# Performance work log

Hardware: AMD Instinct MI355X
Metric: run time of the kernel (lower is better)

## Reference

```python
import jax, jax.numpy as jnp
import numpy as np

N = 2048
D_IN = 128
D_OUT = 128
H = 8
EDGE_DIM = 8
EDGE_HID = 32
NEG_SLOPE = 0.2


def setup_inputs() -> dict:
    key = jax.random.key(0)
    ks = jax.random.split(key, 9)
    return {
        "inputs": jax.random.normal(ks[0], (N, D_IN), dtype=jnp.float32),
        "adj": jax.random.randint(ks[1], (N, N), 0, 2, dtype=jnp.int32),
        "edge_attr": jax.random.normal(ks[2], (N, N, EDGE_DIM), dtype=jnp.float32),
        # Linear weights stored as [in, out] (y = x @ W)
        "Wq": jax.random.normal(ks[3], (D_IN, D_OUT), dtype=jnp.float32) * 0.05,
        "Wk": jax.random.normal(ks[4], (D_IN, D_OUT), dtype=jnp.float32) * 0.05,
        "Wv": jax.random.normal(ks[5], (D_IN, D_OUT), dtype=jnp.float32) * 0.05,
        "We": jax.random.normal(ks[6], (EDGE_DIM, EDGE_HID), dtype=jnp.float32) * 0.05,
        "Wr": jax.random.normal(ks[7], (EDGE_HID, D_OUT), dtype=jnp.float32) * 0.05,
        "Wo": jax.random.normal(ks[8], (D_OUT, D_OUT), dtype=jnp.float32) * 0.05,
    }


def reference(inputs, adj, edge_attr, Wq, Wk, Wv, We, Wr, Wo):
    n = inputs.shape[0]
    dh = D_OUT // H  # head dim = 16
    # Projections -> [H, N, dh]
    Q = (inputs @ Wq).reshape(n, H, dh).transpose(1, 0, 2)
    K = (inputs @ Wk).reshape(n, H, dh).transpose(1, 0, 2)
    V = (inputs @ Wv).reshape(n, H, dh).transpose(1, 0, 2)
    # Edge bias: r_ij = W_r(W_e(e_ij)) viewed per-head; bias_hij = q_hi . r_ijh.
    # Fold We@Wr and contract with Q first to avoid materializing [N,N,D_OUT].
    Wer = (We @ Wr).reshape(EDGE_DIM, H, dh)          # [E, H, dh]
    QW = jnp.einsum('hid,ehd->hie', Q, Wer)           # [H, N, E]
    scores = (jnp.einsum('hid,hjd->hij', Q, K)
              + jnp.einsum('hie,ije->hij', QW, edge_attr)) / jnp.sqrt(jnp.float32(dh))
    scores = jax.nn.leaky_relu(scores, NEG_SLOPE)
    # Adjacency mask: only attend along existing edges
    scores = jnp.where((adj > 0)[None, :, :], scores, jnp.float32(-1e9))
    attn = jax.nn.softmax(scores, axis=-1)            # dropout is identity in eval
    out = jnp.einsum('hij,hjd->hid', attn, V)         # [H, N, dh]
    out = out.transpose(1, 0, 2).reshape(n, D_OUT)
    return out @ Wo
```

## Files before the change

### kernel.cpp

```cpp
#include <hip/hip_runtime.h>
#include <math.h>

#define NN 2048
#define DD 128
#define HH 8
#define DHH 16
#define EDIM 8
#define EHID 32

typedef __attribute__((address_space(1))) const void GV;
typedef __attribute__((address_space(3))) void LV;

__global__ __launch_bounds__(384) void proj_kernel(
    const float* __restrict__ X,
    const float* __restrict__ Wq, const float* __restrict__ Wk,
    const float* __restrict__ Wv, const float* __restrict__ We,
    const float* __restrict__ Wr,
    float* __restrict__ Qo, float* __restrict__ Ko,
    float* __restrict__ Vo, float* __restrict__ QWo) {
  __shared__ float x_lds[2][128];
  __shared__ float wer_lds[8][128];
  __shared__ float q_lds[2][128];
  const int t = threadIdx.x;
  const int i0 = blockIdx.x * 2;

  if (t < 256) x_lds[t >> 7][t & 127] = X[(size_t)i0 * 128 + t];

  if (t < 128) {
    float acc[EDIM];
#pragma unroll
    for (int e = 0; e < EDIM; ++e) acc[e] = 0.f;
    for (int k = 0; k < EHID; ++k) {
      const float wr = Wr[k * 128 + t];
#pragma unroll
      for (int e = 0; e < EDIM; ++e) acc[e] = fmaf(We[e * EHID + k], wr, acc[e]);
    }
#pragma unroll
    for (int e = 0; e < EDIM; ++e) wer_lds[e][t] = acc[e];
  }
  __syncthreads();

  const int mat = t >> 7;
  const int c = t & 127;
  const float* __restrict__ W = (mat == 0) ? Wq : ((mat == 1) ? Wk : Wv);
  float a0 = 0.f, a1 = 0.f;
#pragma unroll 8
  for (int d = 0; d < 128; ++d) {
    const float w = W[d * 128 + c];
    a0 = fmaf(x_lds[0][d], w, a0);
    a1 = fmaf(x_lds[1][d], w, a1);
  }
  float* __restrict__ Out = (mat == 0) ? Qo : ((mat == 1) ? Ko : Vo);
  Out[(size_t)i0 * 128 + c] = a0;
  Out[(size_t)(i0 + 1) * 128 + c] = a1;
  if (mat == 0) { q_lds[0][c] = a0; q_lds[1][c] = a1; }
  __syncthreads();

  if (t < 64) {
    const int h = t >> 3, e = t & 7;
#pragma unroll
    for (int r = 0; r < 2; ++r) {
      float s = 0.f;
#pragma unroll
      for (int d = 0; d < DHH; ++d)
        s = fmaf(q_lds[r][h * DHH + d], wer_lds[e][h * DHH + d], s);
      QWo[(size_t)(i0 + r) * 64 + h * 8 + e] = s;
    }
  }
}

__global__ __launch_bounds__(320) void attn_kernel(
    const float* __restrict__ Qg, const float* __restrict__ Kg,
    const float* __restrict__ Vg, const float* __restrict__ QWg,
    const int* __restrict__ adj, const float* __restrict__ Eg,
    const float* __restrict__ Wo, float* __restrict__ out) {
  __shared__ float4 Ks_lds[4][512];
  __shared__ float4 Vs_lds[4][512];
  __shared__ float4 Es_lds[4][64];
  __shared__ float mbuf[128 * 18];
  __shared__ float o_lds[2][128];

  const int t = threadIdx.x;
  const int i0 = blockIdx.x * 2;

  if (t >= 256) {
    const int lid = t - 256;
    const int hi = lid >> 5;
    const int r = lid & 31;
    const int h_p = r & 7, qq_p = r >> 3;
    const float* Kbase = Kg + (size_t)hi * 16384 + h_p * 16 + qq_p * 4;
    const float* Vbase = Vg + (size_t)hi * 16384 + h_p * 16 + qq_p * 4;
    const int il_e = lid >> 5;
    const int jo_e = (lid & 31) >> 1, half = lid & 1;
    const float* Ebase = Eg + ((size_t)(i0 + il_e) * 2048 + jo_e * 128) * 8 + half * 4;

    auto ISSUE = [&](int slot, int jj) {
      const float* kb = Kbase + (size_t)jj * 128;
      const float* vb = Vbase + (size_t)jj * 128;
      const float* eb = Ebase + (size_t)jj * 8;
#pragma unroll
      for (int j = 0; j < 8; ++j)
        __builtin_amdgcn_global_load_lds((GV*)(kb + j * 32768),
                                         (LV*)&Ks_lds[slot][j * 64], 16, 0, 0);
#pragma unroll
      for (int j = 0; j < 8; ++j)
        __builtin_amdgcn_global_load_lds((GV*)(vb + j * 32768),
                                         (LV*)&Vs_lds[slot][j * 64], 16, 0, 0);
      __builtin_amdgcn_global_load_lds((GV*)eb, (LV*)&Es_lds[slot][0], 16, 0, 0);
    };

    ISSUE(0, 0); ISSUE(1, 1); ISSUE(2, 2);
    asm volatile("s_waitcnt vmcnt(34)" ::: "memory");
    __builtin_amdgcn_s_barrier();
    __builtin_amdgcn_sched_barrier(0);
    for (int jj = 0; jj < 128; ++jj) {
      if (jj < 125) {
        ISSUE((jj + 3) & 3, jj + 3);
        asm volatile("s_waitcnt vmcnt(34)" ::: "memory");
      } else if (jj == 125) {
        asm volatile("s_waitcnt vmcnt(17)" ::: "memory");
      } else {
        asm volatile("s_waitcnt vmcnt(0)" ::: "memory");
      }
      __builtin_amdgcn_s_barrier();
      __builtin_amdgcn_sched_barrier(0);
    }
  } else {
    const int il = t & 1;
    const int h = (t >> 1) & 7;
    const int jo = t >> 4;
    const int i = i0 + il;

    float4 q0, q1, q2, q3, qw0, qw1;
    {
      const float4* qp = (const float4*)(Qg + (size_t)i * 128 + h * 16);
      q0 = qp[0]; q1 = qp[1]; q2 = qp[2]; q3 = qp[3];
      const float4* wp = (const float4*)(QWg + (size_t)i * 64 + h * 8);
      qw0 = wp[0]; qw1 = wp[1];
    }

    float acc[16];
#pragma unroll
    for (int d = 0; d < 16; ++d) acc[d] = 0.f;
    float m = -INFINITY, mt = -INFINITY, l = 0.f;

    const int4* __restrict__ ap4 = (const int4*)(adj + (size_t)i * NN + jo * 128);

    auto score = [&](const float4 E0, const float4 E1,
                     const float4 K0, const float4 K1, const float4 K2,
                     const float4 K3, const int a) -> float {
      float s0 = q0.x * K0.x;    s0 = fmaf(q0.y, K0.y, s0);
      s0 = fmaf(q0.z, K0.z, s0); s0 = fmaf(q0.w, K0.w, s0);
      s0 = fmaf(q1.x, K1.x, s0); s0 = fmaf(q1.y, K1.y, s0);
      s0 = fmaf(q1.z, K1.z, s0); s0 = fmaf(q1.w, K1.w, s0);
      float s1 = q2.x * K2.x;    s1 = fmaf(q2.y, K2.y, s1);
      s1 = fmaf(q2.z, K2.z, s1); s1 = fmaf(q2.w, K2.w, s1);
      s1 = fmaf(q3.x, K3.x, s1); s1 = fmaf(q3.y, K3.y, s1);
      s1 = fmaf(q3.z, K3.z, s1); s1 = fmaf(q3.w, K3.w, s1);
      float b0 = qw0.x * E0.x;    b0 = fmaf(qw0.y, E0.y, b0);
      b0 = fmaf(qw0.z, E0.z, b0); b0 = fmaf(qw0.w, E0.w, b0);
      b0 = fmaf(qw1.x, E1.x, b0); b0 = fmaf(qw1.y, E1.y, b0);
      b0 = fmaf(qw1.z, E1.z, b0); b0 = fmaf(qw1.w, E1.w, b0);
      const float raw = (s0 + s1) + b0;
      float sc2 = fmaf(0.14426950f, fabsf(raw), 0.21640425f * raw);
      sc2 = (a > 0) ? sc2 : -1e9f;
      if (sc2 > mt) {
        const float rr = exp2f(m - sc2);
        l *= rr;
#pragma unroll
        for (int d = 0; d < 16; ++d) acc[d] *= rr;
        m = sc2; mt = sc2 + 12.f;
      }
      const float p = exp2f(sc2 - m);
      l += p;
      return p;
    };
    auto pv = [&](const float p, const float4 V0, const float4 V1,
                  const float4 V2, const float4 V3) {
      acc[0]  = fmaf(p, V0.x, acc[0]);  acc[1]  = fmaf(p, V0.y, acc[1]);
      acc[2]  = fmaf(p, V0.z, acc[2]);  acc[3]  = fmaf(p, V0.w, acc[3]);
      acc[4]  = fmaf(p, V1.x, acc[4]);  acc[5]  = fmaf(p, V1.y, acc[5]);
      acc[6]  = fmaf(p, V1.z, acc[6]);  acc[7]  = fmaf(p, V1.w, acc[7]);
      acc[8]  = fmaf(p, V2.x, acc[8]);  acc[9]  = fmaf(p, V2.y, acc[9]);
      acc[10] = fmaf(p, V2.z, acc[10]); acc[11] = fmaf(p, V2.w, acc[11]);
      acc[12] = fmaf(p, V3.x, acc[12]); acc[13] = fmaf(p, V3.y, acc[13]);
      acc[14] = fmaf(p, V3.z, acc[14]); acc[15] = fmaf(p, V3.w, acc[15]);
    };

    int4 a_cur = ap4[0];
    __builtin_amdgcn_s_barrier();
    __builtin_amdgcn_sched_barrier(0);

    for (int j4 = 0; j4 < 32; ++j4) {
      const int4 a_nxt = ap4[j4 < 31 ? j4 + 1 : 31];
#pragma unroll
      for (int u4 = 0; u4 < 4; ++u4) {
        const int jj = j4 * 4 + u4;
        const int slot = jj & 3;
        const int a = (u4 == 0) ? a_cur.x : (u4 == 1) ? a_cur.y
                    : (u4 == 2) ? a_cur.z : a_cur.w;
        const float4* kq = &Ks_lds[slot][jo * 32 + h];
        const float4 K0 = kq[0], K1 = kq[8], K2 = kq[16], K3 = kq[24];
        const float4* vq = &Vs_lds[slot][jo * 32 + h];
        const float4 V0 = vq[0], V1 = vq[8], V2 = vq[16], V3 = vq[24];
        const float4* eq = &Es_lds[slot][il * 32 + jo * 2];
        const float4 E0 = eq[0], E1 = eq[1];
        const float p = score(E0, E1, K0, K1, K2, K3, a);
        pv(p, V0, V1, V2, V3);
        __builtin_amdgcn_s_barrier();
        __builtin_amdgcn_sched_barrier(0);
      }
      a_cur = a_nxt;
    }

    {
      const int u = t & 15;
      (void)u;
    }
    __syncthreads();
    const int u = t & 15;
    for (int k = 8; k >= 1; k >>= 1) {
      if (jo >= k && jo < 2 * k) {
        float* b = mbuf + ((size_t)((jo - k) * 16 + u)) * 18;
        b[0] = m; b[1] = l;
#pragma unroll
        for (int d = 0; d < 16; ++d) b[2 + d] = acc[d];
      }
      __syncthreads();
      if (jo < k) {
        const float* b = mbuf + ((size_t)(jo * 16 + u)) * 18;
        const float m2 = b[0], l2 = b[1];
        const float M = fmaxf(m, m2);
        const float sa = exp2f(m - M), sb = exp2f(m2 - M);
        l = l * sa + l2 * sb;
#pragma unroll
        for (int d = 0; d < 16; ++d) acc[d] = acc[d] * sa + b[2 + d] * sb;
        m = M;
      }
      __syncthreads();
    }
    if (jo == 0) {
      const float inv = 1.f / l;
#pragma unroll
      for (int d = 0; d < 16; ++d) o_lds[il][h * 16 + d] = acc[d] * inv;
    }
    __syncthreads();
    const int r = t >> 7, c = t & 127;
    float s = 0.f;
#pragma unroll 8
    for (int d = 0; d < 128; ++d)
      s = fmaf(o_lds[r][d], Wo[d * 128 + c], s);
    out[(size_t)(i0 + r) * 128 + c] = s;
    return;
  }

  __syncthreads();
  for (int k = 8; k >= 1; k >>= 1) { __syncthreads(); __syncthreads(); }
  __syncthreads();
}

extern "C" void kernel_launch(void* const* d_in, const int* in_sizes, int n_in,
                              void* d_out, int out_size, void* d_ws, size_t ws_size,
                              hipStream_t stream) {
  const float* X   = (const float*)d_in[0];
  const int*   adj = (const int*)d_in[1];
  const float* E   = (const float*)d_in[2];
  const float* Wq  = (const float*)d_in[3];
  const float* Wk  = (const float*)d_in[4];
  const float* Wv  = (const float*)d_in[5];
  const float* We  = (const float*)d_in[6];
  const float* Wr  = (const float*)d_in[7];
  const float* Wo  = (const float*)d_in[8];
  float* out = (float*)d_out;

  float* Qs  = (float*)d_ws;
  float* Ks  = Qs + (size_t)NN * DD;
  float* Vs  = Ks + (size_t)NN * DD;
  float* QWs = Vs + (size_t)NN * DD;

  hipLaunchKernelGGL(proj_kernel, dim3(NN / 2), dim3(384), 0, stream,
                     X, Wq, Wk, Wv, We, Wr, Qs, Ks, Vs, QWs);
  hipLaunchKernelGGL(attn_kernel, dim3(NN / 2), dim3(320), 0, stream,
                     Qs, Ks, Vs, QWs, adj, E, Wo, out);
}
```

Baseline: 360.7 us.

## Process four query rows per attention block with deeper LDS ring and staged adjacency

The attention kernel now handles four query rows per block instead of two, halving the grid and doubling reuse of each K/V tile staged in LDS. The producer wave group uses a six-slot ring with 256 steps of 8 keys each, and also stages the adjacency row into LDS via direct global-to-LDS loads. Reads are XOR-swizzled to avoid bank conflicts, and the merge and output projection are restructured for the new 8-way key split. This cuts K/V global traffic per query and removes per-thread adjacency loads, at the cost of twice as many barriers per pass and fewer blocks for occupancy.

```diff
diff --git a/kernel.cpp b/kernel.cpp
--- a/kernel.cpp
+++ b/kernel.cpp
@@ -3,13 +3,16 @@
 
 #define NN 2048
 #define DD 128
-#define HH 8
-#define DHH 16
 #define EDIM 8
 #define EHID 32
+#define DHH 16
 
 typedef __attribute__((address_space(1))) const void GV;
 typedef __attribute__((address_space(3))) void LV;
+
+#define NB 6
+#define NSTEP 256
+#define RROWS 4
 
 __global__ __launch_bounds__(384) void proj_kernel(
     const float* __restrict__ X,
@@ -69,98 +72,120 @@
   }
 }
 
+#define DOT4ADD(S, A, B) do {            \
+    S = fmaf((A).x, (B).x, S);           \
+    S = fmaf((A).y, (B).y, S);           \
+    S = fmaf((A).z, (B).z, S);           \
+    S = fmaf((A).w, (B).w, S); } while (0)
+
 __global__ __launch_bounds__(320) void attn_kernel(
     const float* __restrict__ Qg, const float* __restrict__ Kg,
     const float* __restrict__ Vg, const float* __restrict__ QWg,
     const int* __restrict__ adj, const float* __restrict__ Eg,
     const float* __restrict__ Wo, float* __restrict__ out) {
-  __shared__ float4 Ks_lds[4][512];
-  __shared__ float4 Vs_lds[4][512];
-  __shared__ float4 Es_lds[4][64];
-  __shared__ float mbuf[128 * 18];
-  __shared__ float o_lds[2][128];
+  __shared__ float4 KL[NB][256];
+  __shared__ float4 VL[NB][256];
+  __shared__ float4 EL[NB][64];
+  __shared__ int    AL[NB][64];
+  __shared__ float  mbuf[128 * 18];
+  __shared__ float  o_lds[4][128];
 
   const int t = threadIdx.x;
-  const int i0 = blockIdx.x * 2;
+  const int i0 = blockIdx.x * RROWS;
+
+  float acc[16];
+#pragma unroll
+  for (int d = 0; d < 16; ++d) acc[d] = 0.f;
+  float m = -INFINITY, mt = -INFINITY, l = 0.f;
 
   if (t >= 256) {
-    const int lid = t - 256;
-    const int hi = lid >> 5;
-    const int r = lid & 31;
-    const int h_p = r & 7, qq_p = r >> 3;
-    const float* Kbase = Kg + (size_t)hi * 16384 + h_p * 16 + qq_p * 4;
-    const float* Vbase = Vg + (size_t)hi * 16384 + h_p * 16 + qq_p * 4;
-    const int il_e = lid >> 5;
-    const int jo_e = (lid & 31) >> 1, half = lid & 1;
-    const float* Ebase = Eg + ((size_t)(i0 + il_e) * 2048 + jo_e * 128) * 8 + half * 4;
-
-    auto ISSUE = [&](int slot, int jj) {
-      const float* kb = Kbase + (size_t)jj * 128;
-      const float* vb = Vbase + (size_t)jj * 128;
-      const float* eb = Ebase + (size_t)jj * 8;
-#pragma unroll
-      for (int j = 0; j < 8; ++j)
-        __builtin_amdgcn_global_load_lds((GV*)(kb + j * 32768),
-                                         (LV*)&Ks_lds[slot][j * 64], 16, 0, 0);
-#pragma unroll
-      for (int j = 0; j < 8; ++j)
-        __builtin_amdgcn_global_load_lds((GV*)(vb + j * 32768),
-                                         (LV*)&Vs_lds[slot][j * 64], 16, 0, 0);
-      __builtin_amdgcn_global_load_lds((GV*)eb, (LV*)&Es_lds[slot][0], 16, 0, 0);
+    const int ln = t - 256;
+    const float* kS = Kg + (size_t)(ln >> 5) * 128 + (ln & 31) * 4;
+    const float* vS = Vg + (size_t)(ln >> 5) * 128 + (ln & 31) * 4;
+    const float* eS = Eg + ((size_t)(i0 + (ln >> 4)) * NN + ((ln >> 1) & 7)) * 8
+                         + (ln & 1) * 4;
+    const int jsA = ((ln & 15) > 7) ? 7 : (ln & 15);
+    const int* aS = adj + (size_t)(i0 + (ln >> 4)) * NN + jsA;
+
+    auto ISSUE = [&](int sl, int j0) {
+#pragma unroll
+      for (int p = 0; p < 4; ++p)
+        __builtin_amdgcn_global_load_lds((GV*)(kS + (size_t)(j0 + p * 2) * 128),
+                                         (LV*)&KL[sl][p * 64], 16, 0, 0);
+#pragma unroll
+      for (int p = 0; p < 4; ++p)
+        __builtin_amdgcn_global_load_lds((GV*)(vS + (size_t)(j0 + p * 2) * 128),
+                                         (LV*)&VL[sl][p * 64], 16, 0, 0);
+      __builtin_amdgcn_global_load_lds((GV*)(eS + (size_t)j0 * 8),
+                                       (LV*)&EL[sl][0], 16, 0, 0);
+      __builtin_amdgcn_global_load_lds((GV*)(aS + j0), (LV*)&AL[sl][0], 4, 0, 0);
     };
 
-    ISSUE(0, 0); ISSUE(1, 1); ISSUE(2, 2);
-    asm volatile("s_waitcnt vmcnt(34)" ::: "memory");
+    ISSUE(0, 0); ISSUE(1, 8); ISSUE(2, 16); ISSUE(3, 24); ISSUE(4, 32);
+    asm volatile("s_waitcnt vmcnt(40)" ::: "memory");
+    __builtin_amdgcn_sched_barrier(0);
     __builtin_amdgcn_s_barrier();
-    __builtin_amdgcn_sched_barrier(0);
-    for (int jj = 0; jj < 128; ++jj) {
-      if (jj < 125) {
-        ISSUE((jj + 3) & 3, jj + 3);
-        asm volatile("s_waitcnt vmcnt(34)" ::: "memory");
-      } else if (jj == 125) {
-        asm volatile("s_waitcnt vmcnt(17)" ::: "memory");
+
+    int ip = 5, jI = 40;
+    for (int s = 0; s < NSTEP; ++s) {
+      if (s <= 250) {
+        ISSUE(ip, jI);
+        jI += 8;
+        if (++ip == NB) ip = 0;
+        asm volatile("s_waitcnt vmcnt(40)" ::: "memory");
+      } else if (s == 251) {
+        asm volatile("s_waitcnt vmcnt(30)" ::: "memory");
+      } else if (s == 252) {
+        asm volatile("s_waitcnt vmcnt(20)" ::: "memory");
+      } else if (s == 253) {
+        asm volatile("s_waitcnt vmcnt(10)" ::: "memory");
       } else {
         asm volatile("s_waitcnt vmcnt(0)" ::: "memory");
       }
+      __builtin_amdgcn_sched_barrier(0);
       __builtin_amdgcn_s_barrier();
-      __builtin_amdgcn_sched_barrier(0);
     }
   } else {
-    const int il = t & 1;
-    const int h = (t >> 1) & 7;
-    const int jo = t >> 4;
+    const int il = t & 3;
+    const int h = (t >> 2) & 7;
+    const int js = t >> 5;
+    const int hs = (h >> 1) & 3;
+    const int hb = il & 1;
     const int i = i0 + il;
 
-    float4 q0, q1, q2, q3, qw0, qw1;
+    float4 qq0, qq1, qq2, qq3, qw0, qw1;
     {
       const float4* qp = (const float4*)(Qg + (size_t)i * 128 + h * 16);
-      q0 = qp[0]; q1 = qp[1]; q2 = qp[2]; q3 = qp[3];
+      qq0 = qp[0 ^ hs]; qq1 = qp[1 ^ hs]; qq2 = qp[2 ^ hs]; qq3 = qp[3 ^ hs];
       const float4* wp = (const float4*)(QWg + (size_t)i * 64 + h * 8);
-      qw0 = wp[0]; qw1 = wp[1];
-    }
-
-    float acc[16];
-#pragma unroll
-    for (int d = 0; d < 16; ++d) acc[d] = 0.f;
-    float m = -INFINITY, mt = -INFINITY, l = 0.f;
-
-    const int4* __restrict__ ap4 = (const int4*)(adj + (size_t)i * NN + jo * 128);
-
-    auto score = [&](const float4 E0, const float4 E1,
-                     const float4 K0, const float4 K1, const float4 K2,
-                     const float4 K3, const int a) -> float {
-      float s0 = q0.x * K0.x;    s0 = fmaf(q0.y, K0.y, s0);
-      s0 = fmaf(q0.z, K0.z, s0); s0 = fmaf(q0.w, K0.w, s0);
-      s0 = fmaf(q1.x, K1.x, s0); s0 = fmaf(q1.y, K1.y, s0);
-      s0 = fmaf(q1.z, K1.z, s0); s0 = fmaf(q1.w, K1.w, s0);
-      float s1 = q2.x * K2.x;    s1 = fmaf(q2.y, K2.y, s1);
-      s1 = fmaf(q2.z, K2.z, s1); s1 = fmaf(q2.w, K2.w, s1);
-      s1 = fmaf(q3.x, K3.x, s1); s1 = fmaf(q3.y, K3.y, s1);
-      s1 = fmaf(q3.z, K3.z, s1); s1 = fmaf(q3.w, K3.w, s1);
-      float b0 = qw0.x * E0.x;    b0 = fmaf(qw0.y, E0.y, b0);
-      b0 = fmaf(qw0.z, E0.z, b0); b0 = fmaf(qw0.w, E0.w, b0);
-      b0 = fmaf(qw1.x, E1.x, b0); b0 = fmaf(qw1.y, E1.y, b0);
-      b0 = fmaf(qw1.z, E1.z, b0); b0 = fmaf(qw1.w, E1.w, b0);
+      qw0 = wp[0 ^ hb]; qw1 = wp[1 ^ hb];
+    }
+
+    const int kOff = js * 32 + h * 4;
+    const int eOff = il * 16 + js * 2;
+    const int aOff = il * 16 + js;
+
+    __builtin_amdgcn_s_barrier();
+    __builtin_amdgcn_sched_barrier(0);
+
+    int sl = 0;
+    for (int s = 0; s < NSTEP; ++s) {
+      const int a = AL[sl][aOff];
+      const float4 kk0 = KL[sl][kOff + (0 ^ hs)];
+      const float4 kk1 = KL[sl][kOff + (1 ^ hs)];
+      const float4 kk2 = KL[sl][kOff + (2 ^ hs)];
+      const float4 kk3 = KL[sl][kOff + (3 ^ hs)];
+      const float4 ee0 = EL[sl][eOff + (0 ^ hb)];
+      const float4 ee1 = EL[sl][eOff + (1 ^ hb)];
+      const float4 vv0 = VL[sl][kOff + (0 ^ hs)];
+      const float4 vv1 = VL[sl][kOff + (1 ^ hs)];
+      const float4 vv2 = VL[sl][kOff + (2 ^ hs)];
+      const float4 vv3 = VL[sl][kOff + (3 ^ hs)];
+
+      float s0 = 0.f, s1 = 0.f, b0 = 0.f;
+      DOT4ADD(s0, qq0, kk0); DOT4ADD(s0, qq1, kk1);
+      DOT4ADD(s1, qq2, kk2); DOT4ADD(s1, qq3, kk3);
+      DOT4ADD(b0, qw0, ee0); DOT4ADD(b0, qw1, ee1);
       const float raw = (s0 + s1) + b0;
       float sc2 = fmaf(0.14426950f, fabsf(raw), 0.21640425f * raw);
       sc2 = (a > 0) ? sc2 : -1e9f;
@@ -173,90 +198,70 @@
       }
       const float p = exp2f(sc2 - m);
       l += p;
-      return p;
-    };
-    auto pv = [&](const float p, const float4 V0, const float4 V1,
-                  const float4 V2, const float4 V3) {
-      acc[0]  = fmaf(p, V0.x, acc[0]);  acc[1]  = fmaf(p, V0.y, acc[1]);
-      acc[2]  = fmaf(p, V0.z, acc[2]);  acc[3]  = fmaf(p, V0.w, acc[3]);
-      acc[4]  = fmaf(p, V1.x, acc[4]);  acc[5]  = fmaf(p, V1.y, acc[5]);
-      acc[6]  = fmaf(p, V1.z, acc[6]);  acc[7]  = fmaf(p, V1.w, acc[7]);
-      acc[8]  = fmaf(p, V2.x, acc[8]);  acc[9]  = fmaf(p, V2.y, acc[9]);
-      acc[10] = fmaf(p, V2.z, acc[10]); acc[11] = fmaf(p, V2.w, acc[11]);
-      acc[12] = fmaf(p, V3.x, acc[12]); acc[13] = fmaf(p, V3.y, acc[13]);
-      acc[14] = fmaf(p, V3.z, acc[14]); acc[15] = fmaf(p, V3.w, acc[15]);
-    };
-
-    int4 a_cur = ap4[0];
-    __builtin_amdgcn_s_barrier();
-    __builtin_amdgcn_sched_barrier(0);
-
-    for (int j4 = 0; j4 < 32; ++j4) {
-      const int4 a_nxt = ap4[j4 < 31 ? j4 + 1 : 31];
-#pragma unroll
-      for (int u4 = 0; u4 < 4; ++u4) {
-        const int jj = j4 * 4 + u4;
-        const int slot = jj & 3;
-        const int a = (u4 == 0) ? a_cur.x : (u4 == 1) ? a_cur.y
-                    : (u4 == 2) ? a_cur.z : a_cur.w;
-        const float4* kq = &Ks_lds[slot][jo * 32 + h];
-        const float4 K0 = kq[0], K1 = kq[8], K2 = kq[16], K3 = kq[24];
-        const float4* vq = &Vs_lds[slot][jo * 32 + h];
-        const float4 V0 = vq[0], V1 = vq[8], V2 = vq[16], V3 = vq[24];
-        const float4* eq = &Es_lds[slot][il * 32 + jo * 2];
-        const float4 E0 = eq[0], E1 = eq[1];
-        const float p = score(E0, E1, K0, K1, K2, K3, a);
-        pv(p, V0, V1, V2, V3);
-        __builtin_amdgcn_s_barrier();
-        __builtin_amdgcn_sched_barrier(0);
-      }
-      a_cur = a_nxt;
-    }
-
-    {
-      const int u = t & 15;
-      (void)u;
+      acc[0]  = fmaf(p, vv0.x, acc[0]);  acc[1]  = fmaf(p, vv0.y, acc[1]);
+      acc[2]  = fmaf(p, vv0.z, acc[2]);  acc[3]  = fmaf(p, vv0.w, acc[3]);
+      acc[4]  = fmaf(p, vv1.x, acc[4]);  acc[5]  = fmaf(p, vv1.y, acc[5]);
+      acc[6]  = fmaf(p, vv1.z, acc[6]);  acc[7]  = fmaf(p, vv1.w, acc[7]);
+      acc[8]  = fmaf(p, vv2.x, acc[8]);  acc[9]  = fmaf(p, vv2.y, acc[9]);
+      acc[10] = fmaf(p, vv2.z, acc[10]); acc[11] = fmaf(p, vv2.w, acc[11]);
+      acc[12] = fmaf(p, vv3.x, acc[12]); acc[13] = fmaf(p, vv3.y, acc[13]);
+      acc[14] = fmaf(p, vv3.z, acc[14]); acc[15] = fmaf(p, vv3.w, acc[15]);
+
+      __builtin_amdgcn_sched_barrier(0);
+      __builtin_amdgcn_s_barrier();
+      __builtin_amdgcn_sched_barrier(0);
+      if (++sl == NB) sl = 0;
+    }
+  }
+
+  const int ilc = t & 3, hc = (t >> 2) & 7, jsc = t >> 5;
+  const int hsc = (hc >> 1) & 3;
+  const int u = t & 31;
+  for (int k = 4; k >= 1; k >>= 1) {
+    if (t < 256 && jsc >= k && jsc < 2 * k) {
+      float* b = mbuf + ((size_t)((jsc - k) * 32 + u)) * 18;
+      b[0] = m; b[1] = l;
+#pragma unroll
+      for (int d = 0; d < 16; ++d) b[2 + d] = acc[d];
     }
     __syncthreads();
-    const int u = t & 15;
-    for (int k = 8; k >= 1; k >>= 1) {
-      if (jo >= k && jo < 2 * k) {
-        float* b = mbuf + ((size_t)((jo - k) * 16 + u)) * 18;
-        b[0] = m; b[1] = l;
-#pragma unroll
-        for (int d = 0; d < 16; ++d) b[2 + d] = acc[d];
-      }
-      __syncthreads();
-      if (jo < k) {
-        const float* b = mbuf + ((size_t)(jo * 16 + u)) * 18;
-        const float m2 = b[0], l2 = b[1];
-        const float M = fmaxf(m, m2);
-        const float sa = exp2f(m - M), sb = exp2f(m2 - M);
-        l = l * sa + l2 * sb;
-#pragma unroll
-        for (int d = 0; d < 16; ++d) acc[d] = acc[d] * sa + b[2 + d] * sb;
-        m = M;
-      }
-      __syncthreads();
-    }
-    if (jo == 0) {
-      const float inv = 1.f / l;
-#pragma unroll
-      for (int d = 0; d < 16; ++d) o_lds[il][h * 16 + d] = acc[d] * inv;
+    if (t < 256 && jsc < k) {
+      const float* b = mbuf + ((size_t)(jsc * 32 + u)) * 18;
+      const float m2 = b[0], l2 = b[1];
+      const float M = fmaxf(m, m2);
+      const float sa = exp2f(m - M), sb = exp2f(m2 - M);
+      l = l * sa + l2 * sb;
+#pragma unroll
+      for (int d = 0; d < 16; ++d) acc[d] = acc[d] * sa + b[2 + d] * sb;
+      m = M;
     }
     __syncthreads();
-    const int r = t >> 7, c = t & 127;
-    float s = 0.f;
+  }
+  if (t < 256 && jsc == 0) {
+    const float inv = 1.f / l;
+#pragma unroll
+    for (int n = 0; n < 4; ++n) {
+      const int cb = hc * 16 + ((n ^ hsc) << 2);
+      o_lds[ilc][cb + 0] = acc[4 * n + 0] * inv;
+      o_lds[ilc][cb + 1] = acc[4 * n + 1] * inv;
+      o_lds[ilc][cb + 2] = acc[4 * n + 2] * inv;
+      o_lds[ilc][cb + 3] = acc[4 * n + 3] * inv;
+    }
+  }
+  __syncthreads();
+
+  if (t < 256) {
+    const int rr = t >> 7, c = t & 127;
+    float d0 = 0.f, d1 = 0.f;
 #pragma unroll 8
-    for (int d = 0; d < 128; ++d)
-      s = fmaf(o_lds[r][d], Wo[d * 128 + c], s);
-    out[(size_t)(i0 + r) * 128 + c] = s;
-    return;
-  }
-
-  __syncthreads();
-  for (int k = 8; k >= 1; k >>= 1) { __syncthreads(); __syncthreads(); }
-  __syncthreads();
+    for (int d = 0; d < 128; ++d) {
+      const float w = Wo[d * 128 + c];
+      d0 = fmaf(o_lds[rr][d], w, d0);
+      d1 = fmaf(o_lds[rr + 2][d], w, d1);
+    }
+    out[(size_t)(i0 + rr) * 128 + c] = d0;
+    out[(size_t)(i0 + rr + 2) * 128 + c] = d1;
+  }
 }
 
 extern "C" void kernel_launch(void* const* d_in, const int* in_sizes, int n_in,
@@ -280,6 +285,6 @@
 
   hipLaunchKernelGGL(proj_kernel, dim3(NN / 2), dim3(384), 0, stream,
                      X, Wq, Wk, Wv, We, Wr, Qs, Ks, Vs, QWs);
-  hipLaunchKernelGGL(attn_kernel, dim3(NN / 2), dim3(320), 0, stream,
+  hipLaunchKernelGGL(attn_kernel, dim3(NN / RROWS), dim3(320), 0, stream,
                      Qs, Ks, Vs, QWs, adj, E, Wo, out);
 }
```

Result: no change. 367.2 us (+1.8%).
